# Kernel tuning notes

Hardware: AMD Instinct MI355X
Metric: run time of the kernel (lower is better)

## Reference

```python
import jax, jax.numpy as jnp
import numpy as np

N = 100000      # nodes
E = 3200000     # edges
F_IN = 512
HID = 16
C = 10


def setup_inputs() -> dict:
    key = jax.random.key(0)
    k1, k2, k3, k4 = jax.random.split(key, 4)
    x = jax.random.normal(k1, (N, F_IN), dtype=jnp.float32)
    edge_index = jax.random.randint(k2, (2, E), 0, N, dtype=jnp.int64)
    W1 = jax.random.normal(k3, (F_IN, HID), dtype=jnp.float32) * 0.05
    b1 = jnp.zeros((HID,), dtype=jnp.float32)
    W2 = jax.random.normal(k4, (HID, C), dtype=jnp.float32) * 0.05
    b2 = jnp.zeros((C,), dtype=jnp.float32)
    return {"x": x, "edge_index": edge_index, "W1": W1, "b1": b1, "W2": W2, "b2": b2}


def _gcn_norm(edge_index, n):
    # add self-loops, compute symmetric normalization deg^-1/2 * deg^-1/2
    loops = jnp.arange(n, dtype=edge_index.dtype)
    src = jnp.concatenate([edge_index[0], loops])
    dst = jnp.concatenate([edge_index[1], loops])
    deg = jax.ops.segment_sum(jnp.ones_like(dst, dtype=jnp.float32), dst, num_segments=n)
    dinv = jnp.where(deg > 0, jax.lax.rsqrt(deg), 0.0)
    norm = dinv[src] * dinv[dst]  # [E+N]
    return src, dst, norm


def _gcn_layer(h, W, b, src, dst, norm, n):
    h = h @ W                                   # project first (PyG GCNConv)
    msg = h[src] * norm[:, None]                # gather + edge scaling
    agg = jax.ops.segment_sum(msg, dst, num_segments=n)  # scatter-add
    return agg + b


def reference(x, edge_index, W1, b1, W2, b2):
    n = x.shape[0]
    src, dst, norm = _gcn_norm(edge_index, n)
    h = jax.nn.relu(_gcn_layer(x, W1, b1, src, dst, norm, n))
    # F.dropout with training=False is identity (eval mode)
    out = _gcn_layer(h, W2, b2, src, dst, norm, n)
    return jax.nn.log_softmax(out, axis=1)
```

## Files before the change

kernel.cpp:

```cpp
#include <hip/hip_runtime.h>

#define N_NODES 100000
#define N_EDGES 3200000
#define F_IN    512
#define HID     16
#define NCLS    10
#define NB      196
#define EPB     4096
#define TK      32

__global__ __launch_bounds__(256) void k_binit(int* __restrict__ bcntp) {
    int i = blockIdx.x * 256 + threadIdx.x;
    if (i < NB * 16) bcntp[i] = 0;
}

__global__ __launch_bounds__(256) void k_bhist(const int* __restrict__ dst,
                                               int* __restrict__ bcntp) {
    __shared__ int h[256];
    int t = threadIdx.x;
    h[t] = 0;
    __syncthreads();
    int hi = min(N_EDGES, (int)(blockIdx.x + 1) * 8192);
    for (int e = blockIdx.x * 8192 + t; e < hi; e += 256)
        atomicAdd(&h[dst[e] >> 9], 1);
    __syncthreads();
    if (t < NB) {
        int v = h[t];
        if (v) atomicAdd(&bcntp[t * 16], v);
    }
}

__global__ __launch_bounds__(256) void k_bscan(const int* __restrict__ bcntp,
                                               int* __restrict__ boff,
                                               int* __restrict__ bcurp,
                                               int* __restrict__ row) {
    __shared__ int sh[256];
    int t = threadIdx.x;
    int v = (t < NB) ? bcntp[t * 16] : 0;
    sh[t] = v;
    __syncthreads();
    for (int off = 1; off < 256; off <<= 1) {
        int add = (t >= off) ? sh[t - off] : 0;
        __syncthreads();
        sh[t] += add;
        __syncthreads();
    }
    int excl = sh[t] - v;
    if (t < NB) { boff[t] = excl; bcurp[t * 16] = excl; }
    if (t == 0) { boff[NB] = N_EDGES; row[N_NODES] = N_EDGES; }
}

__global__ __launch_bounds__(256) void k_bpart(const int* __restrict__ ei,
                                               int* __restrict__ bcurp,
                                               int* __restrict__ part) {
    __shared__ int cnt_sh[256], base_sh[256];
    int t = threadIdx.x;
    cnt_sh[t] = 0;
    __syncthreads();
    int base = blockIdx.x * EPB;
    int pk[16], bk[16], rk[16];
#pragma unroll
    for (int j = 0; j < 16; ++j) {
        int e = base + j * 256 + t;
        if (e < N_EDGES) {
            int s = ei[e], d = ei[N_EDGES + e];
            bk[j] = d >> 9;
            pk[j] = ((d & 511) << 17) | s;
            rk[j] = atomicAdd(&cnt_sh[bk[j]], 1);
        } else bk[j] = -1;
    }
    __syncthreads();
    if (t < NB && cnt_sh[t] > 0)
        base_sh[t] = atomicAdd(&bcurp[t * 16], cnt_sh[t]);
    __syncthreads();
#pragma unroll
    for (int j = 0; j < 16; ++j)
        if (bk[j] >= 0) part[base_sh[bk[j]] + rk[j]] = pk[j];
}

__global__ __launch_bounds__(256) void k_bucket(const int* __restrict__ boff,
                                                const int* __restrict__ part,
                                                int* __restrict__ row,
                                                float* __restrict__ dinv,
                                                int* __restrict__ srcs) {
    __shared__ int cnt[512], ofs[512], sc[256];
    int t = threadIdx.x;
    int b = blockIdx.x;
    int e0 = boff[b], e1 = boff[b + 1];
    int nbase = b << 9;
    cnt[t] = 0; cnt[t + 256] = 0;
    __syncthreads();
    for (int e = e0 + t; e < e1; e += 256)
        atomicAdd(&cnt[part[e] >> 17], 1);
    __syncthreads();
    int a0 = cnt[2 * t], a1 = cnt[2 * t + 1];
    sc[t] = a0 + a1;
    __syncthreads();
    for (int off = 1; off < 256; off <<= 1) {
        int add = (t >= off) ? sc[t - off] : 0;
        __syncthreads();
        sc[t] += add;
        __syncthreads();
    }
    int excl = sc[t] - (a0 + a1);
    ofs[2 * t] = excl;
    ofs[2 * t + 1] = excl + a0;
    __syncthreads();
#pragma unroll
    for (int r = 0; r < 2; ++r) {
        int ln = t + r * 256;
        int n = nbase + ln;
        if (n < N_NODES) {
            row[n] = e0 + ofs[ln];
            dinv[n] = rsqrtf((float)(cnt[ln] + 1));
        }
    }
    __syncthreads();
    for (int e = e0 + t; e < e1; e += 256) {
        int pp = part[e];
        int pos = atomicAdd(&ofs[pp >> 17], 1);
        srcs[e0 + pos] = pp & 0x1FFFF;
    }
}

__global__ __launch_bounds__(128) void k_gemm1(const float* __restrict__ x,
                                               const float* __restrict__ W1,
                                               const float* __restrict__ dinv,
                                               float* __restrict__ h1s) {
    __shared__ float xs[128][TK + 1];
    const int t = threadIdx.x;
    const int nbase = blockIdx.x * 128;
    const int f4 = t & 7;
    const int r0 = t >> 3;

    float4 pre[8];
#pragma unroll
    for (int p = 0; p < 8; ++p) {
        int n = nbase + r0 + p * 16;
        pre[p] = (n < N_NODES) ? ((const float4*)(x + (size_t)n * F_IN))[f4]
                               : make_float4(0.f, 0.f, 0.f, 0.f);
    }

    float acc[16];
#pragma unroll
    for (int j = 0; j < 16; ++j) acc[j] = 0.f;

    for (int c = 0; c < F_IN; c += TK) {
#pragma unroll
        for (int p = 0; p < 8; ++p) {
            int r = r0 + p * 16;
            xs[r][f4 * 4 + 0] = pre[p].x;
            xs[r][f4 * 4 + 1] = pre[p].y;
            xs[r][f4 * 4 + 2] = pre[p].z;
            xs[r][f4 * 4 + 3] = pre[p].w;
        }
        __syncthreads();
        if (c + TK < F_IN) {
#pragma unroll
            for (int p = 0; p < 8; ++p) {
                int n = nbase + r0 + p * 16;
                pre[p] = (n < N_NODES)
                           ? ((const float4*)(x + (size_t)n * F_IN + c + TK))[f4]
                           : make_float4(0.f, 0.f, 0.f, 0.f);
            }
        }
#pragma unroll
        for (int k = 0; k < TK; ++k) {
            float xv = xs[t][k];
            const float4* wk = (const float4*)(W1 + (c + k) * 16);
            float4 wa = wk[0], wb = wk[1], wc = wk[2], wd = wk[3];
            acc[0]  = fmaf(xv, wa.x, acc[0]);
            acc[1]  = fmaf(xv, wa.y, acc[1]);
            acc[2]  = fmaf(xv, wa.z, acc[2]);
            acc[3]  = fmaf(xv, wa.w, acc[3]);
            acc[4]  = fmaf(xv, wb.x, acc[4]);
            acc[5]  = fmaf(xv, wb.y, acc[5]);
            acc[6]  = fmaf(xv, wb.z, acc[6]);
            acc[7]  = fmaf(xv, wb.w, acc[7]);
            acc[8]  = fmaf(xv, wc.x, acc[8]);
            acc[9]  = fmaf(xv, wc.y, acc[9]);
            acc[10] = fmaf(xv, wc.z, acc[10]);
            acc[11] = fmaf(xv, wc.w, acc[11]);
            acc[12] = fmaf(xv, wd.x, acc[12]);
            acc[13] = fmaf(xv, wd.y, acc[13]);
            acc[14] = fmaf(xv, wd.z, acc[14]);
            acc[15] = fmaf(xv, wd.w, acc[15]);
        }
        __syncthreads();
    }

    int n = nbase + t;
    if (n < N_NODES) {
        float dn = dinv[n];
        float4* o = (float4*)(h1s + (size_t)n * HID);
        o[0] = make_float4(acc[0] * dn,  acc[1] * dn,  acc[2] * dn,  acc[3] * dn);
        o[1] = make_float4(acc[4] * dn,  acc[5] * dn,  acc[6] * dn,  acc[7] * dn);
        o[2] = make_float4(acc[8] * dn,  acc[9] * dn,  acc[10] * dn, acc[11] * dn);
        o[3] = make_float4(acc[12] * dn, acc[13] * dn, acc[14] * dn, acc[15] * dn);
    }
}

__global__ __launch_bounds__(256) void k_edge1g(const int* __restrict__ row,
                                                const int* __restrict__ srcs,
                                                const float* __restrict__ dinv,
                                                const float* __restrict__ h1s,
                                                const float* __restrict__ b1,
                                                float* __restrict__ agg1) {
    int t = blockIdx.x * 256 + threadIdx.x;
    if (t >= N_NODES * HID) return;
    int n = t >> 4, j = t & 15;
    float sum = h1s[t];
    int k = row[n], k1 = row[n + 1];
    for (; k + 4 <= k1; k += 4) {
        int s0 = srcs[k], s1 = srcs[k + 1], s2 = srcs[k + 2], s3 = srcs[k + 3];
        float v0 = h1s[s0 * HID + j], v1 = h1s[s1 * HID + j];
        float v2 = h1s[s2 * HID + j], v3 = h1s[s3 * HID + j];
        sum += (v0 + v1) + (v2 + v3);
    }
    for (; k < k1; ++k) sum += h1s[srcs[k] * HID + j];
    agg1[t] = fmaxf(fmaf(dinv[n], sum, b1[j]), 0.f);
}

__global__ __launch_bounds__(256) void k_gemm2(const float* __restrict__ agg1,
                                               const float* __restrict__ W2,
                                               const float* __restrict__ dinv,
                                               float* __restrict__ ps) {
    int t = blockIdx.x * 256 + threadIdx.x;
    if (t >= N_NODES * NCLS) return;
    int n = t / NCLS, c = t - n * NCLS;
    const float* r = agg1 + n * HID;
    float v = 0.f;
#pragma unroll
    for (int j = 0; j < HID; ++j) v = fmaf(r[j], W2[j * NCLS + c], v);
    ps[t] = v * dinv[n];
}

__global__ __launch_bounds__(256) void k_edge2g(const int* __restrict__ row,
                                                const int* __restrict__ srcs,
                                                const float* __restrict__ dinv,
                                                const float* __restrict__ ps,
                                                const float* __restrict__ b2,
                                                float* __restrict__ out) {
    int t = blockIdx.x * 256 + threadIdx.x;
    if (t >= N_NODES * NCLS) return;
    int n = t / NCLS, c = t - n * NCLS;
    float sum = ps[t];
    int k = row[n], k1 = row[n + 1];
    for (; k + 4 <= k1; k += 4) {
        int s0 = srcs[k], s1 = srcs[k + 1], s2 = srcs[k + 2], s3 = srcs[k + 3];
        float v0 = ps[s0 * NCLS + c], v1 = ps[s1 * NCLS + c];
        float v2 = ps[s2 * NCLS + c], v3 = ps[s3 * NCLS + c];
        sum += (v0 + v1) + (v2 + v3);
    }
    for (; k < k1; ++k) sum += ps[srcs[k] * NCLS + c];
    out[t] = fmaf(dinv[n], sum, b2[c]);
}

__global__ __launch_bounds__(256) void k_lsm(float* __restrict__ out) {
    int n = blockIdx.x * 256 + threadIdx.x;
    if (n >= N_NODES) return;
    float v[NCLS];
    float m = -1e30f;
#pragma unroll
    for (int c = 0; c < NCLS; ++c) {
        v[c] = out[n * NCLS + c];
        m = fmaxf(m, v[c]);
    }
    float s = 0.f;
#pragma unroll
    for (int c = 0; c < NCLS; ++c) s += __expf(v[c] - m);
    float l = __logf(s) + m;
#pragma unroll
    for (int c = 0; c < NCLS; ++c) out[n * NCLS + c] = v[c] - l;
}

extern "C" void kernel_launch(void* const* d_in, const int* in_sizes, int n_in,
                              void* d_out, int out_size, void* d_ws, size_t ws_size,
                              hipStream_t stream) {
    const float* x  = (const float*)d_in[0];
    const int*   ei = (const int*)d_in[1];
    const float* W1 = (const float*)d_in[2];
    const float* b1 = (const float*)d_in[3];
    const float* W2 = (const float*)d_in[4];
    const float* b2 = (const float*)d_in[5];
    float* out = (float*)d_out;

    int* w = (int*)d_ws;
    float* dinv = (float*)w;
    int*   row   = w + 102400;
    int*   bcntp = w + 204816;
    int*   bcurp = w + 207952;
    int*   boff  = w + 211088;
    int*   part  = w + 211344;
    int*   srcs  = w + 3411344;
    float* h1s   = (float*)(w + 6611344);
    float* agg1  = (float*)(w + 8249744);
    float* ps    = h1s;

    k_binit<<<(NB * 16 + 255) / 256, 256, 0, stream>>>(bcntp);
    k_bhist<<<(N_EDGES + 8191) / 8192, 256, 0, stream>>>(ei + N_EDGES, bcntp);
    k_bscan<<<1, 256, 0, stream>>>(bcntp, boff, bcurp, row);
    k_bpart<<<(N_EDGES + EPB - 1) / EPB, 256, 0, stream>>>(ei, bcurp, part);
    k_bucket<<<NB, 256, 0, stream>>>(boff, part, row, dinv, srcs);

    k_gemm1 <<<(N_NODES + 127) / 128, 128, 0, stream>>>(x, W1, dinv, h1s);
    k_edge1g<<<(N_NODES * HID + 255) / 256, 256, 0, stream>>>(row, srcs, dinv, h1s, b1, agg1);
    k_gemm2 <<<(N_NODES * NCLS + 255) / 256, 256, 0, stream>>>(agg1, W2, dinv, ps);
    k_edge2g<<<(N_NODES * NCLS + 255) / 256, 256, 0, stream>>>(row, srcs, dinv, ps, b2, out);
    k_lsm   <<<(N_NODES + 255) / 256, 256, 0, stream>>>(out);
}
```

Measured before the change: 531.0 us.

## Vectorize edge gathers with float4, pad layer-2 rows, fuse log-softmax into aggregation

The layer-1 and layer-2 aggregation kernels now have each thread gather a float4 of neighbor features instead of one float, which cuts index loads and memory transactions by four. Layer-2 projections are stored padded to 12 floats per node in a separate buffer so they can be read as float4. Log-softmax is fused into the layer-2 aggregation using quad shuffles, which removes a kernel launch and a pass over the output. The W1 chunk is also staged in shared memory in gemm1. The price is four times fewer threads per kernel to hide gather latency, plus extra padded reads and stores.

New measurement: 510.2 us. -3.9%, faster.

```diff
diff --git a/kernel.cpp b/kernel.cpp
--- a/kernel.cpp
+++ b/kernel.cpp
@@ -8,6 +8,7 @@
 #define NB      196
 #define EPB     4096
 #define TK      32
+#define PS      12
 
 __global__ __launch_bounds__(256) void k_binit(int* __restrict__ bcntp) {
     int i = blockIdx.x * 256 + threadIdx.x;
@@ -128,6 +129,7 @@
                                                const float* __restrict__ dinv,
                                                float* __restrict__ h1s) {
     __shared__ float xs[128][TK + 1];
+    __shared__ float wchunk[TK * 16];
     const int t = threadIdx.x;
     const int nbase = blockIdx.x * 128;
     const int f4 = t & 7;
@@ -140,6 +142,7 @@
         pre[p] = (n < N_NODES) ? ((const float4*)(x + (size_t)n * F_IN))[f4]
                                : make_float4(0.f, 0.f, 0.f, 0.f);
     }
+    float4 wpre = ((const float4*)W1)[t];
 
     float acc[16];
 #pragma unroll
@@ -154,6 +157,7 @@
             xs[r][f4 * 4 + 2] = pre[p].z;
             xs[r][f4 * 4 + 3] = pre[p].w;
         }
+        ((float4*)wchunk)[t] = wpre;
         __syncthreads();
         if (c + TK < F_IN) {
 #pragma unroll
@@ -163,11 +167,12 @@
                            ? ((const float4*)(x + (size_t)n * F_IN + c + TK))[f4]
                            : make_float4(0.f, 0.f, 0.f, 0.f);
             }
+            wpre = ((const float4*)(W1 + (c + TK) * 16))[t];
         }
 #pragma unroll
         for (int k = 0; k < TK; ++k) {
             float xv = xs[t][k];
-            const float4* wk = (const float4*)(W1 + (c + k) * 16);
+            const float4* wk = (const float4*)&wchunk[k * 16];
             float4 wa = wk[0], wb = wk[1], wc = wk[2], wd = wk[3];
             acc[0]  = fmaf(xv, wa.x, acc[0]);
             acc[1]  = fmaf(xv, wa.y, acc[1]);
@@ -207,18 +212,32 @@
                                                 const float* __restrict__ b1,
                                                 float* __restrict__ agg1) {
     int t = blockIdx.x * 256 + threadIdx.x;
-    if (t >= N_NODES * HID) return;
-    int n = t >> 4, j = t & 15;
-    float sum = h1s[t];
+    if (t >= N_NODES * 4) return;
+    int n = t >> 2, q = t & 3;
+    const float4* h4 = (const float4*)h1s;
+    float4 sum = h4[n * 4 + q];
     int k = row[n], k1 = row[n + 1];
     for (; k + 4 <= k1; k += 4) {
         int s0 = srcs[k], s1 = srcs[k + 1], s2 = srcs[k + 2], s3 = srcs[k + 3];
-        float v0 = h1s[s0 * HID + j], v1 = h1s[s1 * HID + j];
-        float v2 = h1s[s2 * HID + j], v3 = h1s[s3 * HID + j];
-        sum += (v0 + v1) + (v2 + v3);
-    }
-    for (; k < k1; ++k) sum += h1s[srcs[k] * HID + j];
-    agg1[t] = fmaxf(fmaf(dinv[n], sum, b1[j]), 0.f);
+        float4 v0 = h4[s0 * 4 + q], v1 = h4[s1 * 4 + q];
+        float4 v2 = h4[s2 * 4 + q], v3 = h4[s3 * 4 + q];
+        sum.x += (v0.x + v1.x) + (v2.x + v3.x);
+        sum.y += (v0.y + v1.y) + (v2.y + v3.y);
+        sum.z += (v0.z + v1.z) + (v2.z + v3.z);
+        sum.w += (v0.w + v1.w) + (v2.w + v3.w);
+    }
+    for (; k < k1; ++k) {
+        float4 v = h4[srcs[k] * 4 + q];
+        sum.x += v.x; sum.y += v.y; sum.z += v.z; sum.w += v.w;
+    }
+    float dn = dinv[n];
+    float4 bb = ((const float4*)b1)[q];
+    float4 r;
+    r.x = fmaxf(fmaf(dn, sum.x, bb.x), 0.f);
+    r.y = fmaxf(fmaf(dn, sum.y, bb.y), 0.f);
+    r.z = fmaxf(fmaf(dn, sum.z, bb.z), 0.f);
+    r.w = fmaxf(fmaf(dn, sum.w, bb.w), 0.f);
+    ((float4*)agg1)[n * 4 + q] = r;
 }
 
 __global__ __launch_bounds__(256) void k_gemm2(const float* __restrict__ agg1,
@@ -226,13 +245,25 @@
                                                const float* __restrict__ dinv,
                                                float* __restrict__ ps) {
     int t = blockIdx.x * 256 + threadIdx.x;
-    if (t >= N_NODES * NCLS) return;
-    int n = t / NCLS, c = t - n * NCLS;
-    const float* r = agg1 + n * HID;
-    float v = 0.f;
-#pragma unroll
-    for (int j = 0; j < HID; ++j) v = fmaf(r[j], W2[j * NCLS + c], v);
-    ps[t] = v * dinv[n];
+    if (t >= N_NODES * 3) return;
+    int n = t / 3, c4 = t - n * 3;
+    int c0 = c4 * 4;
+    const float4* a4 = (const float4*)(agg1 + n * HID);
+    float4 a0 = a4[0], a1 = a4[1], a2 = a4[2], a3 = a4[3];
+    float aj[16] = {a0.x, a0.y, a0.z, a0.w, a1.x, a1.y, a1.z, a1.w,
+                    a2.x, a2.y, a2.z, a2.w, a3.x, a3.y, a3.z, a3.w};
+    float4 acc = make_float4(0.f, 0.f, 0.f, 0.f);
+#pragma unroll
+    for (int j = 0; j < HID; ++j) {
+        float av = aj[j];
+        acc.x = fmaf(av, W2[j * NCLS + c0], acc.x);
+        acc.y = fmaf(av, W2[j * NCLS + c0 + 1], acc.y);
+        acc.z = fmaf(av, (c0 + 2 < NCLS) ? W2[j * NCLS + c0 + 2] : 0.f, acc.z);
+        acc.w = fmaf(av, (c0 + 3 < NCLS) ? W2[j * NCLS + c0 + 3] : 0.f, acc.w);
+    }
+    float dn = dinv[n];
+    ((float4*)ps)[n * 3 + c4] =
+        make_float4(acc.x * dn, acc.y * dn, acc.z * dn, acc.w * dn);
 }
 
 __global__ __launch_bounds__(256) void k_edge2g(const int* __restrict__ row,
@@ -242,36 +273,48 @@
                                                 const float* __restrict__ b2,
                                                 float* __restrict__ out) {
     int t = blockIdx.x * 256 + threadIdx.x;
-    if (t >= N_NODES * NCLS) return;
-    int n = t / NCLS, c = t - n * NCLS;
-    float sum = ps[t];
+    if (t >= N_NODES * 4) return;
+    int n = t >> 2, q = t & 3;
+    int qc = (q < 3) ? q : 2;
+    const float4* p4 = (const float4*)ps;
+    float4 sum = p4[n * 3 + qc];
     int k = row[n], k1 = row[n + 1];
     for (; k + 4 <= k1; k += 4) {
         int s0 = srcs[k], s1 = srcs[k + 1], s2 = srcs[k + 2], s3 = srcs[k + 3];
-        float v0 = ps[s0 * NCLS + c], v1 = ps[s1 * NCLS + c];
-        float v2 = ps[s2 * NCLS + c], v3 = ps[s3 * NCLS + c];
-        sum += (v0 + v1) + (v2 + v3);
-    }
-    for (; k < k1; ++k) sum += ps[srcs[k] * NCLS + c];
-    out[t] = fmaf(dinv[n], sum, b2[c]);
-}
-
-__global__ __launch_bounds__(256) void k_lsm(float* __restrict__ out) {
-    int n = blockIdx.x * 256 + threadIdx.x;
-    if (n >= N_NODES) return;
-    float v[NCLS];
-    float m = -1e30f;
-#pragma unroll
-    for (int c = 0; c < NCLS; ++c) {
-        v[c] = out[n * NCLS + c];
-        m = fmaxf(m, v[c]);
-    }
-    float s = 0.f;
-#pragma unroll
-    for (int c = 0; c < NCLS; ++c) s += __expf(v[c] - m);
-    float l = __logf(s) + m;
-#pragma unroll
-    for (int c = 0; c < NCLS; ++c) out[n * NCLS + c] = v[c] - l;
+        float4 v0 = p4[s0 * 3 + qc], v1 = p4[s1 * 3 + qc];
+        float4 v2 = p4[s2 * 3 + qc], v3 = p4[s3 * 3 + qc];
+        sum.x += (v0.x + v1.x) + (v2.x + v3.x);
+        sum.y += (v0.y + v1.y) + (v2.y + v3.y);
+        sum.z += (v0.z + v1.z) + (v2.z + v3.z);
+        sum.w += (v0.w + v1.w) + (v2.w + v3.w);
+    }
+    for (; k < k1; ++k) {
+        float4 v = p4[srcs[k] * 3 + qc];
+        sum.x += v.x; sum.y += v.y; sum.z += v.z; sum.w += v.w;
+    }
+    float dn = dinv[n];
+    int c0 = qc * 4;
+    float4 val;
+    val.x = fmaf(dn, sum.x, b2[c0]);
+    val.y = fmaf(dn, sum.y, b2[c0 + 1]);
+    val.z = (c0 + 2 < NCLS) ? fmaf(dn, sum.z, b2[c0 + 2]) : -1e30f;
+    val.w = (c0 + 3 < NCLS) ? fmaf(dn, sum.w, b2[c0 + 3]) : -1e30f;
+    float m = fmaxf(fmaxf(val.x, val.y), fmaxf(val.z, val.w));
+    m = fmaxf(m, __shfl_xor(m, 1));
+    m = fmaxf(m, __shfl_xor(m, 2));
+    float se = __expf(val.x - m) + __expf(val.y - m)
+             + __expf(val.z - m) + __expf(val.w - m);
+    if (q == 3) se = 0.f;
+    se += __shfl_xor(se, 1);
+    se += __shfl_xor(se, 2);
+    float l = m + __logf(se);
+    if (q < 2) {
+        float* o = out + n * NCLS + c0;
+        o[0] = val.x - l; o[1] = val.y - l; o[2] = val.z - l; o[3] = val.w - l;
+    } else if (q == 2) {
+        float* o = out + n * NCLS + 8;
+        o[0] = val.x - l; o[1] = val.y - l;
+    }
 }
 
 extern "C" void kernel_launch(void* const* d_in, const int* in_sizes, int n_in,
@@ -295,7 +338,7 @@
     int*   srcs  = w + 3411344;
     float* h1s   = (float*)(w + 6611344);
     float* agg1  = (float*)(w + 8249744);
-    float* ps    = h1s;
+    float* ps    = (float*)(w + 9888144);
 
     k_binit<<<(NB * 16 + 255) / 256, 256, 0, stream>>>(bcntp);
     k_bhist<<<(N_EDGES + 8191) / 8192, 256, 0, stream>>>(ei + N_EDGES, bcntp);
@@ -304,8 +347,7 @@
     k_bucket<<<NB, 256, 0, stream>>>(boff, part, row, dinv, srcs);
 
     k_gemm1 <<<(N_NODES + 127) / 128, 128, 0, stream>>>(x, W1, dinv, h1s);
-    k_edge1g<<<(N_NODES * HID + 255) / 256, 256, 0, stream>>>(row, srcs, dinv, h1s, b1, agg1);
-    k_gemm2 <<<(N_NODES * NCLS + 255) / 256, 256, 0, stream>>>(agg1, W2, dinv, ps);
-    k_edge2g<<<(N_NODES * NCLS + 255) / 256, 256, 0, stream>>>(row, srcs, dinv, ps, b2, out);
-    k_lsm   <<<(N_NODES + 255) / 256, 256, 0, stream>>>(out);
-}
+    k_edge1g<<<(N_NODES * 4 + 255) / 256, 256, 0, stream>>>(row, srcs, dinv, h1s, b1, agg1);
+    k_gemm2 <<<(N_NODES * 3 + 255) / 256, 256, 0, stream>>>(agg1, W2, dinv, ps);
+    k_edge2g<<<(N_NODES * 4 + 255) / 256, 256, 0, stream>>>(row, srcs, dinv, ps, b2, out);
+}
```
